# Kernel optimization log

Measured on AMD Instinct MI355X. Metric: run time of the kernel, lower is better.

Reference implementation:

```python
import jax, jax.numpy as jnp
import numpy as np


def _rx_gate(weights):
    # Single-qubit Rx gate: cos(w/2) I - i sin(w/2) X  (2x2 complex)
    a = jnp.cos(weights / 2)[0]
    b = jnp.sin(weights / 2)[0]
    eye = jnp.eye(2, dtype=jnp.float32)
    offx = jnp.array([[0.0, 1.0], [1.0, 0.0]], dtype=jnp.float32)
    return (a * eye - 1j * b * offx).astype(jnp.complex64)


def _krons(gate, n_qubits):
    # Recursive Kronecker product of n identical 2x2 gates -> (2^n, 2^n)
    full = gate
    for _ in range(n_qubits - 1):
        full = jnp.kron(full, gate)
    return full


def setup_inputs() -> dict:
    key = jax.random.key(0)
    k1, k2, k3 = jax.random.split(key, 3)
    B, BLK, DC, NQ = 256, 1, 2, 12
    dim = 2 ** NQ  # 4096
    state_re = jax.random.normal(k1, (B, BLK, DC, dim, 1), dtype=jnp.float32)
    state_im = jax.random.normal(k2, (B, BLK, DC, dim, 1), dtype=jnp.float32)
    weights = jax.random.uniform(k3, (1,), dtype=jnp.float32,
                                 minval=-np.pi / 2, maxval=np.pi / 2)
    return {"state_re": state_re, "state_im": state_im,
            "weights": weights, "n_qubits": NQ}


def reference(state_re, state_im, weights, n_qubits):
    gate = _rx_gate(weights)                      # (2, 2) complex64
    full = _krons(gate, n_qubits)                 # (2^n, 2^n) complex64
    state = (state_re + 1j * state_im).astype(jnp.complex64)  # (B,BLK,DC,2^n,1)
    return jnp.matmul(full, state)                # broadcasted dense matmul
```

## Files before the change

### kernel.cpp

```cpp
#include <hip/hip_runtime.h>
#include <hip/hip_bf16.h>


#define DIM 4096
#define TPB 256

__device__ __forceinline__ void bf(float ca, float sb,
                                   float& r0, float& q0, float& r1, float& q1)
{
    const float nr0 = ca * r0 + sb * q1;
    const float nq0 = ca * q0 - sb * r1;
    const float nr1 = ca * r1 + sb * q0;
    const float nq1 = ca * q1 - sb * r0;
    r0 = nr0; q0 = nq0; r1 = nr1; q1 = nq1;
}

template <bool INTERLEAVED>
__global__ __launch_bounds__(TPB) void rx_layer_kernel(
    const float* __restrict__ re, const float* __restrict__ im,
    const float* __restrict__ w, float* __restrict__ out)
{
    __shared__ float lds[32][TPB];

    const int v = blockIdx.x;
    const int t = threadIdx.x;

    const float4* re4 = (const float4*)(re + (size_t)v * DIM);
    const float4* im4 = (const float4*)(im + (size_t)v * DIM);

    float r[4][4], q[4][4];
#pragma unroll
    for (int h = 0; h < 4; ++h) {
        const float4 a = re4[256 * h + t];
        const float4 b = im4[256 * h + t];
        r[h][0] = a.x; r[h][1] = a.y; r[h][2] = a.z; r[h][3] = a.w;
        q[h][0] = b.x; q[h][1] = b.y; q[h][2] = b.z; q[h][3] = b.w;
    }

    const float half = 0.5f * w[0];
    const float ca = cosf(half);
    const float sb = sinf(half);

#pragma unroll
    for (int h = 0; h < 4; ++h) {
        bf(ca, sb, r[h][0], q[h][0], r[h][1], q[h][1]);
        bf(ca, sb, r[h][2], q[h][2], r[h][3], q[h][3]);
        bf(ca, sb, r[h][0], q[h][0], r[h][2], q[h][2]);
        bf(ca, sb, r[h][1], q[h][1], r[h][3], q[h][3]);
    }
#pragma unroll
    for (int c = 0; c < 4; ++c) {
        bf(ca, sb, r[0][c], q[0][c], r[1][c], q[1][c]);
        bf(ca, sb, r[2][c], q[2][c], r[3][c], q[3][c]);
        bf(ca, sb, r[0][c], q[0][c], r[2][c], q[2][c]);
        bf(ca, sb, r[1][c], q[1][c], r[3][c], q[3][c]);
    }

#pragma unroll
    for (int s = 0; s < 6; ++s) {
        const int m = 1 << s;
#pragma unroll
        for (int h = 0; h < 4; ++h)
#pragma unroll
            for (int c = 0; c < 4; ++c) {
                const float rp = __shfl_xor(r[h][c], m, 64);
                const float qp = __shfl_xor(q[h][c], m, 64);
                r[h][c] = ca * r[h][c] + sb * qp;
                q[h][c] = ca * q[h][c] - sb * rp;
            }
    }

    const int wv = t >> 6;
    const int l  = t & 63;
#pragma unroll
    for (int h = 0; h < 4; ++h)
#pragma unroll
        for (int c = 0; c < 4; ++c) {
            const int k = (h * 4 + c) * 2;
            lds[k + 0][t] = r[h][c];
            lds[k + 1][t] = q[h][c];
        }
    __syncthreads();

    const float A2 = ca * ca;
    const float AB = ca * sb;
    const float B2 = sb * sb;
    const int p1 = ((wv ^ 1) << 6) | l;
    const int p2 = ((wv ^ 2) << 6) | l;
    const int p3 = ((wv ^ 3) << 6) | l;

#pragma unroll
    for (int h = 0; h < 4; ++h)
#pragma unroll
        for (int c = 0; c < 4; ++c) {
            const int k = (h * 4 + c) * 2;
            const float r1 = lds[k][p1],     r2 = lds[k][p2],     r3 = lds[k][p3];
            const float q1 = lds[k + 1][p1], q2 = lds[k + 1][p2], q3 = lds[k + 1][p3];
            const float nr = A2 * r[h][c] + AB * (q1 + q2) - B2 * r3;
            const float nq = A2 * q[h][c] - AB * (r1 + r2) - B2 * q3;
            r[h][c] = nr;
            q[h][c] = nq;
        }

    if (INTERLEAVED) {
        float* o = out + (size_t)v * DIM * 2;
#pragma unroll
        for (int h = 0; h < 4; ++h) {
            float4* o4 = (float4*)(o + 2048 * h + 8 * t);
            o4[0] = make_float4(r[h][0], q[h][0], r[h][1], q[h][1]);
            o4[1] = make_float4(r[h][2], q[h][2], r[h][3], q[h][3]);
        }
    } else {
        float4* o4 = (float4*)(out + (size_t)v * DIM);
#pragma unroll
        for (int h = 0; h < 4; ++h)
            o4[256 * h + t] = make_float4(r[h][0], r[h][1], r[h][2], r[h][3]);
    }
}

extern "C" void kernel_launch(void* const* d_in, const int* in_sizes, int n_in,
                              void* d_out, int out_size, void* d_ws, size_t ws_size,
                              hipStream_t stream)
{
    const float* re = (const float*)d_in[0];
    const float* im = (const float*)d_in[1];
    const float* w  = (const float*)d_in[2];
    float* out = (float*)d_out;

    const int nvec = in_sizes[0] / DIM;

    if (out_size == 2 * in_sizes[0]) {
        rx_layer_kernel<true><<<nvec, TPB, 0, stream>>>(re, im, w, out);
    } else {
        rx_layer_kernel<false><<<nvec, TPB, 0, stream>>>(re, im, w, out);
    }
}
```

Baseline: 76.20 us.

## Replace shuffle stages with LDS transposes using XOR-swizzled shared buffers

Replaces the six warp-shuffle butterfly stages and the cross-wave LDS combine with two LDS transposes. Each thread gathers 16 elements and applies four register-local butterfly stages per pass, using XOR-swizzled float2 buffers to avoid bank conflicts. This removes the many shuffle instructions, but the output stores become strided float2 or float writes instead of float4, and LDS use grows to 64KB per block, which may lower occupancy.

```diff
diff --git a/kernel.cpp b/kernel.cpp
--- a/kernel.cpp
+++ b/kernel.cpp
@@ -4,6 +4,8 @@
 
 #define DIM 4096
 #define TPB 256
+
+__device__ __forceinline__ int sig(int j) { return j ^ ((j >> 6) & 15); }
 
 __device__ __forceinline__ void bf(float ca, float sb,
                                    float& r0, float& q0, float& r1, float& q1)
@@ -20,7 +22,8 @@
     const float* __restrict__ re, const float* __restrict__ im,
     const float* __restrict__ w, float* __restrict__ out)
 {
-    __shared__ float lds[32][TPB];
+    __shared__ float2 buf0[DIM];
+    __shared__ float2 buf1[DIM];
 
     const int v = blockIdx.x;
     const int t = threadIdx.x;
@@ -57,64 +60,59 @@
     }
 
 #pragma unroll
-    for (int s = 0; s < 6; ++s) {
+    for (int h = 0; h < 4; ++h)
+#pragma unroll
+        for (int c = 0; c < 4; ++c)
+            buf0[sig(1024 * h + 4 * t + c)] = make_float2(r[h][c], q[h][c]);
+    __syncthreads();
+
+    const int baseB = ((t >> 6) << 10) | (((t >> 2) & 15) << 6) | (t & 3);
+    float rb[16], qb[16];
+#pragma unroll
+    for (int e = 0; e < 16; ++e) {
+        const float2 x = buf0[sig(baseB + (e << 2))];
+        rb[e] = x.x; qb[e] = x.y;
+    }
+#pragma unroll
+    for (int s = 0; s < 4; ++s) {
         const int m = 1 << s;
 #pragma unroll
-        for (int h = 0; h < 4; ++h)
-#pragma unroll
-            for (int c = 0; c < 4; ++c) {
-                const float rp = __shfl_xor(r[h][c], m, 64);
-                const float qp = __shfl_xor(q[h][c], m, 64);
-                r[h][c] = ca * r[h][c] + sb * qp;
-                q[h][c] = ca * q[h][c] - sb * rp;
-            }
+        for (int i = 0; i < 16; ++i)
+            if (!(i & m))
+                bf(ca, sb, rb[i], qb[i], rb[i | m], qb[i | m]);
     }
 
-    const int wv = t >> 6;
-    const int l  = t & 63;
 #pragma unroll
-    for (int h = 0; h < 4; ++h)
-#pragma unroll
-        for (int c = 0; c < 4; ++c) {
-            const int k = (h * 4 + c) * 2;
-            lds[k + 0][t] = r[h][c];
-            lds[k + 1][t] = q[h][c];
-        }
+    for (int e = 0; e < 16; ++e)
+        buf1[sig(baseB + (e << 2))] = make_float2(rb[e], qb[e]);
     __syncthreads();
 
-    const float A2 = ca * ca;
-    const float AB = ca * sb;
-    const float B2 = sb * sb;
-    const int p1 = ((wv ^ 1) << 6) | l;
-    const int p2 = ((wv ^ 2) << 6) | l;
-    const int p3 = ((wv ^ 3) << 6) | l;
-
+    const int baseC = ((t >> 6) << 10) | (((t >> 2) & 15) << 2) | (t & 3);
+    float rc[16], qc[16];
 #pragma unroll
-    for (int h = 0; h < 4; ++h)
+    for (int f = 0; f < 16; ++f) {
+        const float2 x = buf1[sig(baseC + (f << 6))];
+        rc[f] = x.x; qc[f] = x.y;
+    }
 #pragma unroll
-        for (int c = 0; c < 4; ++c) {
-            const int k = (h * 4 + c) * 2;
-            const float r1 = lds[k][p1],     r2 = lds[k][p2],     r3 = lds[k][p3];
-            const float q1 = lds[k + 1][p1], q2 = lds[k + 1][p2], q3 = lds[k + 1][p3];
-            const float nr = A2 * r[h][c] + AB * (q1 + q2) - B2 * r3;
-            const float nq = A2 * q[h][c] - AB * (r1 + r2) - B2 * q3;
-            r[h][c] = nr;
-            q[h][c] = nq;
-        }
+    for (int s = 0; s < 4; ++s) {
+        const int m = 1 << s;
+#pragma unroll
+        for (int i = 0; i < 16; ++i)
+            if (!(i & m))
+                bf(ca, sb, rc[i], qc[i], rc[i | m], qc[i | m]);
+    }
 
     if (INTERLEAVED) {
-        float* o = out + (size_t)v * DIM * 2;
+        float2* o2 = (float2*)out + (size_t)v * DIM;
 #pragma unroll
-        for (int h = 0; h < 4; ++h) {
-            float4* o4 = (float4*)(o + 2048 * h + 8 * t);
-            o4[0] = make_float4(r[h][0], q[h][0], r[h][1], q[h][1]);
-            o4[1] = make_float4(r[h][2], q[h][2], r[h][3], q[h][3]);
-        }
+        for (int f = 0; f < 16; ++f)
+            o2[baseC + (f << 6)] = make_float2(rc[f], qc[f]);
     } else {
-        float4* o4 = (float4*)(out + (size_t)v * DIM);
+        float* o = out + (size_t)v * DIM + baseC;
 #pragma unroll
-        for (int h = 0; h < 4; ++h)
-            o4[256 * h + t] = make_float4(r[h][0], r[h][1], r[h][2], r[h][3]);
+        for (int f = 0; f < 16; ++f)
+            o[f << 6] = rc[f];
     }
 }
 
```

Result: no change. 75.69 us (-0.7%).
